# Performance work log

Hardware: AMD Instinct MI355X
Metric: run time of the kernel (lower is better)

Reference implementation:

```python
import jax, jax.numpy as jnp
from jax import lax
import numpy as np

B, L, E, D, A, M, V, T = 64, 196, 2048, 512, 512, 512, 30000, 21


def setup_inputs() -> dict:
    key = jax.random.key(0)
    ks = jax.random.split(key, 22)
    s = 0.02
    encoder_out = jax.random.normal(ks[0], (B, L, E), jnp.float32)
    captions = jax.random.randint(ks[1], (B, T), 0, V, dtype=jnp.int32)
    lens = jax.random.randint(ks[2], (B,), 2, T + 1, dtype=jnp.int32)
    caption_lengths = jnp.sort(lens)[::-1]  # descending, as torch loop requires
    p = {
        'W_enc': jax.random.normal(ks[3], (E, A)) * s, 'b_enc': jnp.zeros((A,)),
        'W_dec': jax.random.normal(ks[4], (D, A)) * s, 'b_dec': jnp.zeros((A,)),
        'w_att': jax.random.normal(ks[5], (A, 1)) * s, 'b_att': jnp.zeros((1,)),
        'emb': jax.random.uniform(ks[6], (V, M), minval=-0.1, maxval=0.1),
        'W_ih': jax.random.normal(ks[7], (M + E, 4 * D)) * s, 'b_ih': jnp.zeros((4 * D,)),
        'W_hh': jax.random.normal(ks[8], (D, 4 * D)) * s, 'b_hh': jnp.zeros((4 * D,)),
        'W_h0': jax.random.normal(ks[9], (E, D)) * s, 'b_h0': jnp.zeros((D,)),
        'W_c0': jax.random.normal(ks[10], (E, D)) * s, 'b_c0': jnp.zeros((D,)),
        'W_beta': jax.random.normal(ks[11], (D, E)) * s, 'b_beta': jnp.zeros((E,)),
        'W_fc': jax.random.uniform(ks[12], (D, V), minval=-0.1, maxval=0.1), 'b_fc': jnp.zeros((V,)),
    }
    return {'encoder_out': encoder_out, 'captions': captions,
            'caption_lengths': caption_lengths, **p}


def reference(encoder_out, captions, caption_lengths,
              W_enc, b_enc, W_dec, b_dec, w_att, b_att, emb,
              W_ih, b_ih, W_hh, b_hh, W_h0, b_h0, W_c0, b_c0,
              W_beta, b_beta, W_fc, b_fc):
    max_len = captions.shape[1] - 1  # teacher forcing: predict y_1..y_T
    x_emb = emb[captions]            # [B,T,M]  (dropout = identity in eval)

    mean_enc = encoder_out.mean(axis=1)
    h0 = jnp.tanh(mean_enc @ W_h0 + b_h0)
    c0 = jnp.tanh(mean_enc @ W_c0 + b_c0)

    # enc projection is constant across timesteps -> hoist out of the loop
    e_proj = encoder_out @ W_enc + b_enc  # [B,L,A]

    # mask[b,t] = (caption_lengths[b]-1) > t  (valid only because lens sorted desc,
    # matching the torch batch_t truncation exactly)
    mask = (caption_lengths[:, None] - 1) > jnp.arange(max_len)[None, :]

    def step(carry, xs):
        h, c = carry
        emb_t, m = xs  # [B,M], [B]
        d = h @ W_dec + b_dec                                   # [B,A]
        energy = (jax.nn.relu(e_proj + d[:, None, :]) @ w_att)[..., 0] + b_att[0]  # [B,L]
        alpha = jax.nn.softmax(energy, axis=1)
        ctx = jnp.einsum('ble,bl->be', encoder_out, alpha)      # [B,E]
        gate = jax.nn.sigmoid(h @ W_beta + b_beta)
        x = jnp.concatenate([emb_t, gate * ctx], axis=1)        # [B,M+E]
        gates = x @ W_ih + b_ih + h @ W_hh + b_hh               # [B,4D]
        i, f, g, o = jnp.split(gates, 4, axis=1)
        c_new = jax.nn.sigmoid(f) * c + jax.nn.sigmoid(i) * jnp.tanh(g)
        h_new = jax.nn.sigmoid(o) * jnp.tanh(c_new)
        pred = h_new @ W_fc + b_fc                              # [B,V]
        mf = m[:, None].astype(pred.dtype)
        return (h_new, c_new), (pred * mf, alpha * mf)

    xs = (jnp.swapaxes(x_emb[:, :max_len, :], 0, 1), mask.T)    # time-major
    _, (preds, alphas) = lax.scan(step, (h0, c0), xs)
    predictions = jnp.swapaxes(preds, 0, 1)                     # [B,max_len,V]
    alphas = jnp.swapaxes(alphas, 0, 1)                         # [B,max_len,L]
    return predictions, alphas
```

## Files before the change

### kernel.cpp

```cpp
#include <hip/hip_runtime.h>
#include <math.h>

namespace {

constexpr int NB  = 64;
constexpr int NL  = 196;
constexpr int NE  = 2048;
constexpr int ND  = 512;
constexpr int NA  = 512;
constexpr int NM  = 512;
constexpr int NV  = 30000;
constexpr int NT  = 21;
constexpr int NML = 20;
constexpr int NG  = 4 * ND;
constexpr int KXG = NM + NE + ND;
constexpr int KSPL = 8, KSL = KXG / KSPL;
constexpr int NALL = ND + NE + NV;
constexpr int OFF_GATE = ND;
constexpr int OFF_PRED = ND + NE;

constexpr size_t WS_MEAN = 0;
constexpr size_t WS_C0   = WS_MEAN + (size_t)NB * NE;
constexpr size_t WS_C1   = WS_C0   + (size_t)NB * ND;
constexpr size_t WS_D    = WS_C1   + (size_t)NB * ND;
constexpr size_t WS_GATE = WS_D    + (size_t)NB * NA;
constexpr size_t WS_EN   = WS_GATE + (size_t)NB * NE;
constexpr size_t WS_CNT  = WS_EN   + (size_t)NB * NL;
constexpr size_t WS_PP   = WS_CNT  + 64;
constexpr size_t WS_SHB  = WS_PP   + (size_t)1048576;
constexpr size_t SH_HB0  = 0;
constexpr size_t SH_HB1  = SH_HB0  + (size_t)NB * ND;
constexpr size_t SH_XEMB = SH_HB1  + (size_t)NB * ND;
constexpr size_t SH_GCTX = SH_XEMB + (size_t)NML * NB * NM;
constexpr size_t SH_EPROJ= SH_GCTX + (size_t)NB * NE;
constexpr size_t SH_WET  = SH_EPROJ+ (size_t)NB * NL * NA;
constexpr size_t SH_WIHX = SH_WET  + (size_t)NA * NE;
constexpr size_t SH_WALL = SH_WIHX + (size_t)NG * KXG;
constexpr size_t SH_ENCBF= SH_WALL + (size_t)NALL * ND;
constexpr size_t SH_END  = SH_ENCBF+ (size_t)NB * NL * NE;
constexpr size_t BYTES_ENC = WS_SHB * 4 + SH_END * 2;

typedef __attribute__((ext_vector_type(8))) short short8v;
typedef __attribute__((ext_vector_type(4))) float f32x4;

__device__ __forceinline__ float sigmoidf_(float x) { return 1.f / (1.f + expf(-x)); }
__device__ __forceinline__ short f2bf(float f) {
  unsigned u = __float_as_uint(f);
  return (short)((u + 0x7FFFu + ((u >> 16) & 1u)) >> 16);
}
__device__ __forceinline__ float bf2f(short s) {
  return __uint_as_float(((unsigned)(unsigned short)s) << 16);
}


__device__ __forceinline__ void gload16(const short* g, short* l) {
  __builtin_amdgcn_global_load_lds(
      (const __attribute__((address_space(1))) unsigned int*)(g),
      (__attribute__((address_space(3))) unsigned int*)(l), 16, 0, 0);
}

template <int R>
__device__ __forceinline__ void stage_direct(const short* __restrict__ src, int ldK,
                                             int rowClamp, short* lds, int tid) {
  int wv = tid >> 6, lane = tid & 63;
  int sub = lane >> 3;
  int kb  = (lane & 7) ^ sub;
#pragma unroll
  for (int g = wv; g < R / 8; g += 4) {
    int row = g * 8 + sub;
    int r = row < rowClamp ? row : rowClamp;
    gload16(src + (size_t)r * ldK + (kb << 3), lds + g * 512);
  }
}

template <int R>
__device__ __forceinline__ void stage_f32cvt(const float* __restrict__ src, int ldK,
                                             short* lds, int tid) {
#pragma unroll
  for (int cidx = tid; cidx < R * 8; cidx += 256) {
    int row = cidx >> 3, kb = cidx & 7;
    const float* p = src + (size_t)row * ldK + kb * 8;
    float4 x = *(const float4*)p;
    float4 y = *(const float4*)(p + 4);
    short8v s;
    s[0] = f2bf(x.x); s[1] = f2bf(x.y); s[2] = f2bf(x.z); s[3] = f2bf(x.w);
    s[4] = f2bf(y.x); s[5] = f2bf(y.y); s[6] = f2bf(y.z); s[7] = f2bf(y.w);
    *(short8v*)(lds + row * 64 + ((kb ^ (row & 7)) << 3)) = s;
  }
}

template <int FM, int FN>
__device__ __forceinline__ void mma_tiles(const short* ldsA, const short* ldsB,
                                          int wr, int wc, int lane, f32x4 acc[FM][FN]) {
  int l15 = lane & 15;
#pragma unroll
  for (int kk = 0; kk < 2; ++kk) {
    int kb0 = kk * 4 + (lane >> 4);
    short8v a[FM], b[FN];
#pragma unroll
    for (int m = 0; m < FM; ++m) {
      int row = wr * FM * 16 + m * 16 + l15;
      a[m] = *(const short8v*)(ldsA + row * 64 + ((kb0 ^ (row & 7)) << 3));
    }
#pragma unroll
    for (int n = 0; n < FN; ++n) {
      int row = wc * FN * 16 + n * 16 + l15;
      b[n] = *(const short8v*)(ldsB + row * 64 + ((kb0 ^ (row & 7)) << 3));
    }
#pragma unroll
    for (int m = 0; m < FM; ++m)
#pragma unroll
      for (int n = 0; n < FN; ++n)
        acc[m][n] = __builtin_amdgcn_mfma_f32_16x16x32_bf16(a[m], b[n], acc[m][n], 0, 0, 0);
  }
}


template <bool PERM>
__global__ __launch_bounds__(256) void k_tcvt(const float* __restrict__ src, int Ks, int Ns,
                                              short* __restrict__ dst, int ldDst, int kOff) {
  __shared__ float tbuf[32][33];
  int n0 = blockIdx.x * 32, k0 = blockIdx.y * 32;
  int tx = threadIdx.x, ty = threadIdx.y;
#pragma unroll
  for (int i = 0; i < 32; i += 8) {
    int k = k0 + ty + i, n = n0 + tx;
    tbuf[ty + i][tx] = (k < Ks && n < Ns) ? src[(size_t)k * Ns + n] : 0.f;
  }
  __syncthreads();
#pragma unroll
  for (int i = 0; i < 32; i += 8) {
    int n = n0 + ty + i, k = k0 + tx;
    if (n < Ns && k < Ks) {
      int nd = PERM ? (((n & 511) << 2) | (n >> 9)) : n;
      dst[(size_t)nd * ldDst + kOff + k] = f2bf(tbuf[tx][ty + i]);
    }
  }
}

template <bool BF>
__global__ __launch_bounds__(256) void k_prep(const float* __restrict__ enc,
                                              short* __restrict__ encbf,
                                              float* __restrict__ mean_enc) {
  int b = blockIdx.y;
  int e = blockIdx.x * 256 + threadIdx.x;
  const float* p = enc + (size_t)b * NL * NE + e;
  short* q = encbf + (size_t)b * NL * NE + e;
  float s = 0.f;
  for (int l = 0; l < NL; ++l) {
    float v = p[(size_t)l * NE];
    s += v;
    if (BF) q[(size_t)l * NE] = f2bf(v);
  }
  mean_enc[(size_t)b * NE + e] = s * (1.f / NL);
}

__global__ void k_xemb(const int* __restrict__ caps, const float* __restrict__ emb,
                       short* __restrict__ xemb) {
  int i = blockIdx.x * 256 + threadIdx.x;
  int m = i & (NM - 1), b = (i >> 9) & (NB - 1), t = i >> 15;
  xemb[i] = f2bf(emb[(size_t)caps[b * NT + t] * NM + m]);
}

__global__ void k_init0(const float* __restrict__ mean_enc, const float* __restrict__ W_h0,
                        const float* __restrict__ W_c0, float* __restrict__ PP) {
  int idx = blockIdx.x * 256 + threadIdx.x;
  int ks = blockIdx.y;
  int b = idx >> 10, jh = idx & 1023, half = jh >> 9, j = jh & 511;
  const float* W = half ? W_c0 : W_h0;
  const float* mp = mean_enc + (size_t)b * NE + ks * 128;
  const float* Wp = W + (size_t)(ks * 128) * ND + j;
  float acc = 0.f;
#pragma unroll 4
  for (int k = 0; k < 128; ++k) acc = fmaf(mp[k], Wp[(size_t)k * ND], acc);
  PP[(size_t)ks * 65536 + idx] = acc;
}

__global__ void k_init1(const float* __restrict__ PP, const float* __restrict__ b_h0,
                        const float* __restrict__ b_c0, float* __restrict__ c0,
                        short* __restrict__ hb0) {
  int idx = blockIdx.x * 256 + threadIdx.x;
  int b = idx >> 9, j = idx & 511;
  float ah = b_h0[j], ac = b_c0[j];
  for (int s = 0; s < 16; ++s) {
    const float* p = PP + (size_t)s * 65536 + b * 1024;
    ah += p[j]; ac += p[512 + j];
  }
  c0[idx] = tanhf(ac);
  hb0[idx] = f2bf(tanhf(ah));
}

template <bool BF>
__global__ __launch_bounds__(256) void k_eproj(const float* __restrict__ enc,
                                               const short* __restrict__ encbf,
                                               const short* __restrict__ We_t,
                                               const float* __restrict__ b_enc,
                                               short* __restrict__ e_proj) {
  constexpr int FM = 4, FN = 4;
  __shared__ short ldsA[128 * 64], ldsB[128 * 64];
  int p = blockIdx.x;
  int l = (p & 7) * 49 + (p >> 3);
  int bn = (l & 3) * 128, bm = (l >> 2) * 128;
  int tid = threadIdx.x, lane = tid & 63, wave = tid >> 6, wr = wave >> 1, wc = wave & 1;
  f32x4 acc[FM][FN];
#pragma unroll
  for (int m = 0; m < FM; ++m)
#pragma unroll
    for (int n = 0; n < FN; ++n) acc[m][n] = (f32x4){0.f, 0.f, 0.f, 0.f};
  for (int k0 = 0; k0 < NE; k0 += 64) {
    __syncthreads();
    if (BF) stage_direct<128>(encbf + (size_t)bm * NE + k0, NE, 127, ldsA, tid);
    else    stage_f32cvt<128>(enc + (size_t)bm * NE + k0, NE, ldsA, tid);
    stage_direct<128>(We_t + (size_t)bn * NE + k0, NE, 127, ldsB, tid);
    __syncthreads();
    mma_tiles<FM, FN>(ldsA, ldsB, wr, wc, lane, acc);
  }
#pragma unroll
  for (int m = 0; m < FM; ++m)
#pragma unroll
    for (int n = 0; n < FN; ++n) {
      int col = bn + wc * FN * 16 + n * 16 + (lane & 15);
      float bias = b_enc[col];
#pragma unroll
      for (int r = 0; r < 4; ++r) {
        int row = bm + wr * FM * 16 + m * 16 + (lane >> 4) * 4 + r;
        e_proj[(size_t)row * NA + col] = f2bf(acc[m][n][r] + bias);
      }
    }
}

__global__ __launch_bounds__(256) void k_hgemm(const short* __restrict__ h_bf,
                                               const short* __restrict__ Wall_t,
                                               const float* __restrict__ b_dec,
                                               const float* __restrict__ b_beta,
                                               const float* __restrict__ b_fc,
                                               const int* __restrict__ clen,
                                               float* __restrict__ d_buf,
                                               float* __restrict__ gatebuf,
                                               float* __restrict__ preds, int t) {
  constexpr int FM = 2, FN = 2;
  __shared__ short ldsA[64 * 64], ldsB[64 * 64];
  int bn = blockIdx.x * 64;
  int tid = threadIdx.x, lane = tid & 63, wave = tid >> 6, wr = wave >> 1, wc = wave & 1;
  int rowClampB = NALL - 1 - bn; if (rowClampB > 63) rowClampB = 63;
  f32x4 acc[FM][FN];
#pragma unroll
  for (int m = 0; m < FM; ++m)
#pragma unroll
    for (int n = 0; n < FN; ++n) acc[m][n] = (f32x4){0.f, 0.f, 0.f, 0.f};
  for (int k0 = 0; k0 < ND; k0 += 64) {
    __syncthreads();
    stage_direct<64>(h_bf + k0, ND, 63, ldsA, tid);
    stage_direct<64>(Wall_t + (size_t)bn * ND + k0, ND, rowClampB, ldsB, tid);
    __syncthreads();
    mma_tiles<FM, FN>(ldsA, ldsB, wr, wc, lane, acc);
  }
#pragma unroll
  for (int m = 0; m < FM; ++m)
#pragma unroll
    for (int r = 0; r < 4; ++r) {
      int row = wr * FM * 16 + m * 16 + (lane >> 4) * 4 + r;
      float mf = ((clen[row] - 1) > t) ? 1.f : 0.f;
#pragma unroll
      for (int n = 0; n < FN; ++n) {
        int col = bn + wc * FN * 16 + n * 16 + (lane & 15);
        float a = acc[m][n][r];
        if (bn < OFF_GATE) {
          d_buf[(size_t)row * NA + col] = a + b_dec[col];
        } else if (bn < OFF_PRED) {
          int e = col - OFF_GATE;
          gatebuf[(size_t)row * NE + e] = sigmoidf_(a + b_beta[e]);
        } else {
          int v = col - OFF_PRED;
          if (v < NV) preds[((size_t)row * NML + t) * NV + v] = mf * (a + b_fc[v]);
        }
      }
    }
}


__global__ __launch_bounds__(256) void k_energy(const short* __restrict__ e_proj,
                                                const float* __restrict__ d_buf,
                                                const float* __restrict__ w_att,
                                                const float* __restrict__ b_att,
                                                float* __restrict__ energy) {
  int tid = threadIdx.x, wave = tid >> 6, lane = tid & 63;
  int row = blockIdx.x * 4 + wave;
  int b = row / NL;
  short8v ev = *(const short8v*)(e_proj + (size_t)row * NA + lane * 8);
  const float* dp = d_buf + (size_t)b * NA + lane * 8;
  float4 d0 = *(const float4*)dp, d1 = *(const float4*)(dp + 4);
  const float* wp = w_att + lane * 8;
  float4 w0 = *(const float4*)wp, w1 = *(const float4*)(wp + 4);
  float dd[8] = {d0.x, d0.y, d0.z, d0.w, d1.x, d1.y, d1.z, d1.w};
  float ww[8] = {w0.x, w0.y, w0.z, w0.w, w1.x, w1.y, w1.z, w1.w};
  float acc = 0.f;
#pragma unroll
  for (int i = 0; i < 8; ++i) {
    float v = bf2f(ev[i]) + dd[i];
    acc = fmaf(fmaxf(v, 0.f), ww[i], acc);
  }
#pragma unroll
  for (int off = 32; off; off >>= 1) acc += __shfl_down(acc, off);
  if (lane == 0) energy[row] = acc + b_att[0];
}

template <bool BF>
__global__ __launch_bounds__(256) void k_ctx(const short* __restrict__ encbf,
                                             const float* __restrict__ encf,
                                             const float* __restrict__ energy,
                                             const float* __restrict__ gatebuf,
                                             const int* __restrict__ clen,
                                             short* __restrict__ gctx,
                                             float* __restrict__ alphas_out, int t) {
  int b = blockIdx.y, e0 = blockIdx.x * 512, tid = threadIdx.x;
  __shared__ float al[NL];
  __shared__ float red[8];
  int wave = tid >> 6, lane = tid & 63;
  float v = (tid < NL) ? energy[b * NL + tid] : -INFINITY;
  float mx = v;
#pragma unroll
  for (int off = 32; off; off >>= 1) mx = fmaxf(mx, __shfl_down(mx, off));
  if (lane == 0) red[wave] = mx;
  __syncthreads();
  if (tid == 0) red[0] = fmaxf(fmaxf(red[0], red[1]), fmaxf(red[2], red[3]));
  __syncthreads();
  mx = red[0];
  float ex = (tid < NL) ? expf(v - mx) : 0.f;
  float sm = ex;
#pragma unroll
  for (int off = 32; off; off >>= 1) sm += __shfl_down(sm, off);
  if (lane == 0) red[4 + wave] = sm;
  __syncthreads();
  if (tid == 0) red[0] = 1.f / (red[4] + red[5] + red[6] + red[7]);
  __syncthreads();
  float alv = ex * red[0];
  if (tid < NL) {
    al[tid] = alv;
    if (blockIdx.x == 0) {
      float mf = ((clen[b] - 1) > t) ? 1.f : 0.f;
      alphas_out[((size_t)b * NML + t) * NL + tid] = alv * mf;
    }
  }
  __syncthreads();
  float cx0 = 0.f, cx1 = 0.f;
  if (BF) {
    const unsigned* p = (const unsigned*)(encbf + (size_t)b * NL * NE + e0) + tid;
#pragma unroll 4
    for (int l = 0; l < NL; ++l) {
      unsigned u = p[(size_t)l * (NE / 2)];
      cx0 = fmaf(al[l], bf2f((short)(u & 0xffffu)), cx0);
      cx1 = fmaf(al[l], bf2f((short)(u >> 16)), cx1);
    }
  } else {
    const float* p = encf + (size_t)b * NL * NE + e0 + 2 * tid;
#pragma unroll 4
    for (int l = 0; l < NL; ++l) {
      float2 u = *(const float2*)(p + (size_t)l * NE);
      cx0 = fmaf(al[l], u.x, cx0);
      cx1 = fmaf(al[l], u.y, cx1);
    }
  }
  int e = e0 + 2 * tid;
  const float* gp = gatebuf + (size_t)b * NE + e;
  unsigned out = (unsigned)(unsigned short)f2bf(cx0 * gp[0]) |
                 ((unsigned)(unsigned short)f2bf(cx1 * gp[1]) << 16);
  *(unsigned*)(gctx + (size_t)b * NE + e) = out;
}

__global__ __launch_bounds__(256) void k_gates(const short* __restrict__ xemb_t,
                                               const short* __restrict__ gctx,
                                               const short* __restrict__ h_prev,
                                               const short* __restrict__ Wihx_t,
                                               float* __restrict__ P) {
  constexpr int FM = 2, FN = 2;
  __shared__ short ldsA[64 * 64], ldsB[64 * 64];
  int bn = blockIdx.x * 64, ks = blockIdx.y;
  int tid = threadIdx.x, lane = tid & 63, wave = tid >> 6, wr = wave >> 1, wc = wave & 1;
  f32x4 acc[FM][FN];
#pragma unroll
  for (int m = 0; m < FM; ++m)
#pragma unroll
    for (int n = 0; n < FN; ++n) acc[m][n] = (f32x4){0.f, 0.f, 0.f, 0.f};
  int kend = (ks + 1) * KSL;
  for (int k0 = ks * KSL; k0 < kend; k0 += 64) {
    const short* asrc; int aldk;
    if (k0 < NM)           { asrc = xemb_t + k0;              aldk = NM; }
    else if (k0 < NM + NE) { asrc = gctx + (k0 - NM);         aldk = NE; }
    else                   { asrc = h_prev + (k0 - NM - NE);  aldk = ND; }
    __syncthreads();
    stage_direct<64>(asrc, aldk, 63, ldsA, tid);
    stage_direct<64>(Wihx_t + (size_t)bn * KXG + k0, KXG, 63, ldsB, tid);
    __syncthreads();
    mma_tiles<FM, FN>(ldsA, ldsB, wr, wc, lane, acc);
  }
#pragma unroll
  for (int m = 0; m < FM; ++m)
#pragma unroll
    for (int n = 0; n < FN; ++n) {
      int col = bn + wc * FN * 16 + n * 16 + (lane & 15);
#pragma unroll
      for (int r = 0; r < 4; ++r) {
        int row = wr * FM * 16 + m * 16 + (lane >> 4) * 4 + r;
        P[((size_t)ks * NB + row) * NG + col] = acc[m][n][r];
      }
    }
}

__global__ void k_lstm(const float* __restrict__ P, const float* __restrict__ b_ih,
                       const float* __restrict__ b_hh, const float* __restrict__ c_prev,
                       float* __restrict__ c_next, short* __restrict__ h_next) {
  int idx = blockIdx.x * 256 + threadIdx.x;
  int b = idx >> 9, j = idx & (ND - 1);
  float gi = b_ih[j] + b_hh[j];
  float gf = b_ih[j + ND] + b_hh[j + ND];
  float gg = b_ih[j + 2 * ND] + b_hh[j + 2 * ND];
  float go = b_ih[j + 3 * ND] + b_hh[j + 3 * ND];
#pragma unroll
  for (int s = 0; s < KSPL; ++s) {
    float4 v = *(const float4*)&P[((size_t)s * NB + b) * NG + j * 4];
    gi += v.x; gf += v.y; gg += v.z; go += v.w;
  }
  float cn = sigmoidf_(gf) * c_prev[idx] + sigmoidf_(gi) * tanhf(gg);
  float hn = sigmoidf_(go) * tanhf(cn);
  c_next[idx] = cn;
  h_next[idx] = f2bf(hn);
}

}

extern "C" void kernel_launch(void* const* d_in, const int* in_sizes, int n_in,
                              void* d_out, int out_size, void* d_ws, size_t ws_size,
                              hipStream_t stream) {
  (void)in_sizes; (void)n_in; (void)out_size;
  const float* enc    = (const float*)d_in[0];
  const int*   caps   = (const int*)d_in[1];
  const int*   clen   = (const int*)d_in[2];
  const float* W_enc  = (const float*)d_in[3];
  const float* b_enc  = (const float*)d_in[4];
  const float* W_dec  = (const float*)d_in[5];
  const float* b_dec  = (const float*)d_in[6];
  const float* w_att  = (const float*)d_in[7];
  const float* b_att  = (const float*)d_in[8];
  const float* emb    = (const float*)d_in[9];
  const float* W_ih   = (const float*)d_in[10];
  const float* b_ih   = (const float*)d_in[11];
  const float* W_hh   = (const float*)d_in[12];
  const float* b_hh   = (const float*)d_in[13];
  const float* W_h0   = (const float*)d_in[14];
  const float* b_h0   = (const float*)d_in[15];
  const float* W_c0   = (const float*)d_in[16];
  const float* b_c0   = (const float*)d_in[17];
  const float* W_beta = (const float*)d_in[18];
  const float* b_beta = (const float*)d_in[19];
  const float* W_fc   = (const float*)d_in[20];
  const float* b_fc   = (const float*)d_in[21];

  float* ws     = (float*)d_ws;
  float* preds  = (float*)d_out;
  float* alphas = preds + (size_t)NB * NML * NV;

  float* mean_enc = ws + WS_MEAN;
  float* cbuf[2]  = {ws + WS_C0, ws + WS_C1};
  float* d_buf    = ws + WS_D;
  float* gatebuf  = ws + WS_GATE;
  float* energy   = ws + WS_EN;
  float* PP       = ws + WS_PP;
  short* shb      = (short*)(ws + WS_SHB);
  short* hbuf[2]  = {shb + SH_HB0, shb + SH_HB1};
  short* xemb     = shb + SH_XEMB;
  short* gctx     = shb + SH_GCTX;
  short* e_proj   = shb + SH_EPROJ;
  short* We_t     = shb + SH_WET;
  short* Wihx_t   = shb + SH_WIHX;
  short* Wall_t   = shb + SH_WALL;
  short* encbf    = shb + SH_ENCBF;
  const bool use_bf = ws_size >= BYTES_ENC;

  k_tcvt<false><<<dim3(NA / 32, NE / 32), dim3(32, 8), 0, stream>>>(W_enc, NE, NA, We_t, NE, 0);
  k_tcvt<true><<<dim3(NG / 32, (NM + NE) / 32), dim3(32, 8), 0, stream>>>(
      W_ih, NM + NE, NG, Wihx_t, KXG, 0);
  k_tcvt<true><<<dim3(NG / 32, ND / 32), dim3(32, 8), 0, stream>>>(
      W_hh, ND, NG, Wihx_t, KXG, NM + NE);
  k_tcvt<false><<<dim3(NA / 32, ND / 32), dim3(32, 8), 0, stream>>>(W_dec, ND, NA, Wall_t, ND, 0);
  k_tcvt<false><<<dim3(NE / 32, ND / 32), dim3(32, 8), 0, stream>>>(
      W_beta, ND, NE, Wall_t + (size_t)OFF_GATE * ND, ND, 0);
  k_tcvt<false><<<dim3((NV + 31) / 32, ND / 32), dim3(32, 8), 0, stream>>>(
      W_fc, ND, NV, Wall_t + (size_t)OFF_PRED * ND, ND, 0);
  if (use_bf)
    k_prep<true><<<dim3(NE / 256, NB), 256, 0, stream>>>(enc, encbf, mean_enc);
  else
    k_prep<false><<<dim3(NE / 256, NB), 256, 0, stream>>>(enc, encbf, mean_enc);
  k_xemb<<<(NML * NB * NM) / 256, 256, 0, stream>>>(caps, emb, xemb);

  k_init0<<<dim3(256, 16), 256, 0, stream>>>(mean_enc, W_h0, W_c0, PP);
  k_init1<<<(NB * ND) / 256, 256, 0, stream>>>(PP, b_h0, b_c0, cbuf[0], hbuf[0]);
  if (use_bf)
    k_eproj<true><<<392, 256, 0, stream>>>(enc, encbf, We_t, b_enc, e_proj);
  else
    k_eproj<false><<<392, 256, 0, stream>>>(enc, encbf, We_t, b_enc, e_proj);
  k_hgemm<<<OFF_PRED / 64, 256, 0, stream>>>(hbuf[0], Wall_t, b_dec, b_beta, b_fc, clen,
                                             d_buf, gatebuf, preds, 0);

  for (int t = 0; t < NML; ++t) {
    short* h_prev = hbuf[t & 1];
    short* h_next = hbuf[1 - (t & 1)];
    float* c_prev = cbuf[t & 1];
    float* c_next = cbuf[1 - (t & 1)];
    k_energy<<<(NB * NL) / 4, 256, 0, stream>>>(e_proj, d_buf, w_att, b_att, energy);
    if (use_bf)
      k_ctx<true><<<dim3(NE / 512, NB), 256, 0, stream>>>(encbf, enc, energy, gatebuf,
                                                          clen, gctx, alphas, t);
    else
      k_ctx<false><<<dim3(NE / 512, NB), 256, 0, stream>>>(encbf, enc, energy, gatebuf,
                                                           clen, gctx, alphas, t);
    k_gates<<<dim3(NG / 64, KSPL), 256, 0, stream>>>(xemb + (size_t)t * NB * NM, gctx,
                                                     h_prev, Wihx_t, PP);
    k_lstm<<<(NB * ND) / 256, 256, 0, stream>>>(PP, b_ih, b_hh, c_prev, c_next, h_next);
    k_hgemm<<<(NALL + 63) / 64, 256, 0, stream>>>(h_next, Wall_t, b_dec, b_beta, b_fc,
                                                  clen, d_buf, gatebuf, preds, t);
  }
}
```

Measured before the change: 1.157 ms.

## Batch vocab projection across timesteps and fold h·W_hh into hidden GEMM

All hidden states are now stored in one buffer, so the 30000-wide output projection runs once after the loop as a single 1280-row GEMM with 128x128 tiles. Previously it ran every timestep with only 64 rows. The h·W_hh product moves out of the split-K gates GEMM into the per-step hidden GEMM, alongside the decoder and beta projections, and is added in the LSTM cell kernel. This makes the W_fc weight reads far more reusable and shrinks the recurrent critical path. The cost is more workspace for the stored hidden states and a separate transposed W_fc buffer.

```diff
diff --git a/kernel.cpp b/kernel.cpp
--- a/kernel.cpp
+++ b/kernel.cpp
@@ -13,30 +13,30 @@
 constexpr int NT  = 21;
 constexpr int NML = 20;
 constexpr int NG  = 4 * ND;
-constexpr int KXG = NM + NE + ND;
+constexpr int KXG = NM + NE;
 constexpr int KSPL = 8, KSL = KXG / KSPL;
-constexpr int NALL = ND + NE + NV;
+constexpr int NDG = ND + NE + NG;
 constexpr int OFF_GATE = ND;
-constexpr int OFF_PRED = ND + NE;
+constexpr int OFF_HWHH = ND + NE;
 
 constexpr size_t WS_MEAN = 0;
 constexpr size_t WS_C0   = WS_MEAN + (size_t)NB * NE;
 constexpr size_t WS_C1   = WS_C0   + (size_t)NB * ND;
 constexpr size_t WS_D    = WS_C1   + (size_t)NB * ND;
 constexpr size_t WS_GATE = WS_D    + (size_t)NB * NA;
-constexpr size_t WS_EN   = WS_GATE + (size_t)NB * NE;
-constexpr size_t WS_CNT  = WS_EN   + (size_t)NB * NL;
-constexpr size_t WS_PP   = WS_CNT  + 64;
+constexpr size_t WS_HWHH = WS_GATE + (size_t)NB * NE;
+constexpr size_t WS_EN   = WS_HWHH + (size_t)NB * NG;
+constexpr size_t WS_PP   = WS_EN   + (size_t)NB * NL;
 constexpr size_t WS_SHB  = WS_PP   + (size_t)1048576;
-constexpr size_t SH_HB0  = 0;
-constexpr size_t SH_HB1  = SH_HB0  + (size_t)NB * ND;
-constexpr size_t SH_XEMB = SH_HB1  + (size_t)NB * ND;
+constexpr size_t SH_HALL = 0;
+constexpr size_t SH_XEMB = SH_HALL + (size_t)(NML + 1) * NB * ND;
 constexpr size_t SH_GCTX = SH_XEMB + (size_t)NML * NB * NM;
 constexpr size_t SH_EPROJ= SH_GCTX + (size_t)NB * NE;
 constexpr size_t SH_WET  = SH_EPROJ+ (size_t)NB * NL * NA;
 constexpr size_t SH_WIHX = SH_WET  + (size_t)NA * NE;
 constexpr size_t SH_WALL = SH_WIHX + (size_t)NG * KXG;
-constexpr size_t SH_ENCBF= SH_WALL + (size_t)NALL * ND;
+constexpr size_t SH_WFC  = SH_WALL + (size_t)NDG * ND;
+constexpr size_t SH_ENCBF= SH_WFC  + (size_t)NV * ND;
 constexpr size_t SH_END  = SH_ENCBF+ (size_t)NB * NL * NE;
 constexpr size_t BYTES_ENC = WS_SHB * 4 + SH_END * 2;
 
@@ -178,7 +178,7 @@
 
 __global__ void k_init1(const float* __restrict__ PP, const float* __restrict__ b_h0,
                         const float* __restrict__ b_c0, float* __restrict__ c0,
-                        short* __restrict__ hb0) {
+                        short* __restrict__ h0) {
   int idx = blockIdx.x * 256 + threadIdx.x;
   int b = idx >> 9, j = idx & 511;
   float ah = b_h0[j], ac = b_c0[j];
@@ -187,7 +187,7 @@
     ah += p[j]; ac += p[512 + j];
   }
   c0[idx] = tanhf(ac);
-  hb0[idx] = f2bf(tanhf(ah));
+  h0[idx] = f2bf(tanhf(ah));
 }
 
 template <bool BF>
@@ -229,20 +229,17 @@
     }
 }
 
-__global__ __launch_bounds__(256) void k_hgemm(const short* __restrict__ h_bf,
-                                               const short* __restrict__ Wall_t,
-                                               const float* __restrict__ b_dec,
-                                               const float* __restrict__ b_beta,
-                                               const float* __restrict__ b_fc,
-                                               const int* __restrict__ clen,
-                                               float* __restrict__ d_buf,
-                                               float* __restrict__ gatebuf,
-                                               float* __restrict__ preds, int t) {
+__global__ __launch_bounds__(256) void k_hgemm_dg(const short* __restrict__ h_bf,
+                                                  const short* __restrict__ Wall_t,
+                                                  const float* __restrict__ b_dec,
+                                                  const float* __restrict__ b_beta,
+                                                  float* __restrict__ d_buf,
+                                                  float* __restrict__ gatebuf,
+                                                  float* __restrict__ hWhh) {
   constexpr int FM = 2, FN = 2;
   __shared__ short ldsA[64 * 64], ldsB[64 * 64];
   int bn = blockIdx.x * 64;
   int tid = threadIdx.x, lane = tid & 63, wave = tid >> 6, wr = wave >> 1, wc = wave & 1;
-  int rowClampB = NALL - 1 - bn; if (rowClampB > 63) rowClampB = 63;
   f32x4 acc[FM][FN];
 #pragma unroll
   for (int m = 0; m < FM; ++m)
@@ -251,7 +248,7 @@
   for (int k0 = 0; k0 < ND; k0 += 64) {
     __syncthreads();
     stage_direct<64>(h_bf + k0, ND, 63, ldsA, tid);
-    stage_direct<64>(Wall_t + (size_t)bn * ND + k0, ND, rowClampB, ldsB, tid);
+    stage_direct<64>(Wall_t + (size_t)bn * ND + k0, ND, 63, ldsB, tid);
     __syncthreads();
     mma_tiles<FM, FN>(ldsA, ldsB, wr, wc, lane, acc);
   }
@@ -260,19 +257,17 @@
 #pragma unroll
     for (int r = 0; r < 4; ++r) {
       int row = wr * FM * 16 + m * 16 + (lane >> 4) * 4 + r;
-      float mf = ((clen[row] - 1) > t) ? 1.f : 0.f;
 #pragma unroll
       for (int n = 0; n < FN; ++n) {
         int col = bn + wc * FN * 16 + n * 16 + (lane & 15);
         float a = acc[m][n][r];
         if (bn < OFF_GATE) {
           d_buf[(size_t)row * NA + col] = a + b_dec[col];
-        } else if (bn < OFF_PRED) {
+        } else if (bn < OFF_HWHH) {
           int e = col - OFF_GATE;
           gatebuf[(size_t)row * NE + e] = sigmoidf_(a + b_beta[e]);
         } else {
-          int v = col - OFF_PRED;
-          if (v < NV) preds[((size_t)row * NML + t) * NV + v] = mf * (a + b_fc[v]);
+          hWhh[(size_t)row * NG + (col - OFF_HWHH)] = a;
         }
       }
     }
@@ -370,7 +365,6 @@
 
 __global__ __launch_bounds__(256) void k_gates(const short* __restrict__ xemb_t,
                                                const short* __restrict__ gctx,
-                                               const short* __restrict__ h_prev,
                                                const short* __restrict__ Wihx_t,
                                                float* __restrict__ P) {
   constexpr int FM = 2, FN = 2;
@@ -385,9 +379,8 @@
   int kend = (ks + 1) * KSL;
   for (int k0 = ks * KSL; k0 < kend; k0 += 64) {
     const short* asrc; int aldk;
-    if (k0 < NM)           { asrc = xemb_t + k0;              aldk = NM; }
-    else if (k0 < NM + NE) { asrc = gctx + (k0 - NM);         aldk = NE; }
-    else                   { asrc = h_prev + (k0 - NM - NE);  aldk = ND; }
+    if (k0 < NM) { asrc = xemb_t + k0;      aldk = NM; }
+    else         { asrc = gctx + (k0 - NM); aldk = NE; }
     __syncthreads();
     stage_direct<64>(asrc, aldk, 63, ldsA, tid);
     stage_direct<64>(Wihx_t + (size_t)bn * KXG + k0, KXG, 63, ldsB, tid);
@@ -407,15 +400,17 @@
     }
 }
 
-__global__ void k_lstm(const float* __restrict__ P, const float* __restrict__ b_ih,
-                       const float* __restrict__ b_hh, const float* __restrict__ c_prev,
-                       float* __restrict__ c_next, short* __restrict__ h_next) {
+__global__ void k_lstm(const float* __restrict__ P, const float* __restrict__ hWhh,
+                       const float* __restrict__ b_ih, const float* __restrict__ b_hh,
+                       const float* __restrict__ c_prev, float* __restrict__ c_next,
+                       short* __restrict__ h_next) {
   int idx = blockIdx.x * 256 + threadIdx.x;
   int b = idx >> 9, j = idx & (ND - 1);
-  float gi = b_ih[j] + b_hh[j];
-  float gf = b_ih[j + ND] + b_hh[j + ND];
-  float gg = b_ih[j + 2 * ND] + b_hh[j + 2 * ND];
-  float go = b_ih[j + 3 * ND] + b_hh[j + 3 * ND];
+  float4 hw = *(const float4*)&hWhh[(size_t)b * NG + j * 4];
+  float gi = b_ih[j] + b_hh[j] + hw.x;
+  float gf = b_ih[j + ND] + b_hh[j + ND] + hw.y;
+  float gg = b_ih[j + 2 * ND] + b_hh[j + 2 * ND] + hw.z;
+  float go = b_ih[j + 3 * ND] + b_hh[j + 3 * ND] + hw.w;
 #pragma unroll
   for (int s = 0; s < KSPL; ++s) {
     float4 v = *(const float4*)&P[((size_t)s * NB + b) * NG + j * 4];
@@ -425,6 +420,52 @@
   float hn = sigmoidf_(go) * tanhf(cn);
   c_next[idx] = cn;
   h_next[idx] = f2bf(hn);
+}
+
+__global__ __launch_bounds__(256) void k_pred(const short* __restrict__ h_all1,
+                                              const short* __restrict__ Wfc_t,
+                                              const float* __restrict__ b_fc,
+                                              const int* __restrict__ clen,
+                                              float* __restrict__ preds) {
+  constexpr int FM = 4, FN = 4;
+  constexpr int NT_M = 10, NT_N = (NV + 127) / 128;
+  constexpr int TOT = NT_M * NT_N;
+  __shared__ short ldsA[128 * 64], ldsB[128 * 64];
+  int p = blockIdx.x;
+  int q = TOT / 8, r8 = TOT % 8;
+  int xcd = p & 7, i = p >> 3;
+  int l = (xcd < r8 ? xcd * (q + 1) : r8 * (q + 1) + (xcd - r8) * q) + i;
+  int bm = (l % NT_M) * 128, bn = (l / NT_M) * 128;
+  int tid = threadIdx.x, lane = tid & 63, wave = tid >> 6, wr = wave >> 1, wc = wave & 1;
+  int rowClampB = NV - 1 - bn; if (rowClampB > 127) rowClampB = 127;
+  f32x4 acc[FM][FN];
+#pragma unroll
+  for (int m = 0; m < FM; ++m)
+#pragma unroll
+    for (int n = 0; n < FN; ++n) acc[m][n] = (f32x4){0.f, 0.f, 0.f, 0.f};
+  for (int k0 = 0; k0 < ND; k0 += 64) {
+    __syncthreads();
+    stage_direct<128>(h_all1 + (size_t)bm * ND + k0, ND, 127, ldsA, tid);
+    stage_direct<128>(Wfc_t + (size_t)bn * ND + k0, ND, rowClampB, ldsB, tid);
+    __syncthreads();
+    mma_tiles<FM, FN>(ldsA, ldsB, wr, wc, lane, acc);
+  }
+#pragma unroll
+  for (int m = 0; m < FM; ++m)
+#pragma unroll
+    for (int n = 0; n < FN; ++n) {
+      int col = bn + wc * FN * 16 + n * 16 + (lane & 15);
+      if (col < NV) {
+        float bias = b_fc[col];
+#pragma unroll
+        for (int r = 0; r < 4; ++r) {
+          int row = bm + wr * FM * 16 + m * 16 + (lane >> 4) * 4 + r;
+          int t = row >> 6, b = row & 63;
+          float mf = ((clen[b] - 1) > t) ? 1.f : 0.f;
+          preds[((size_t)b * NML + t) * NV + col] = mf * (acc[m][n][r] + bias);
+        }
+      }
+    }
 }
 
 }
@@ -464,29 +505,31 @@
   float* cbuf[2]  = {ws + WS_C0, ws + WS_C1};
   float* d_buf    = ws + WS_D;
   float* gatebuf  = ws + WS_GATE;
+  float* hWhh     = ws + WS_HWHH;
   float* energy   = ws + WS_EN;
   float* PP       = ws + WS_PP;
   short* shb      = (short*)(ws + WS_SHB);
-  short* hbuf[2]  = {shb + SH_HB0, shb + SH_HB1};
+  short* h_all    = shb + SH_HALL;
   short* xemb     = shb + SH_XEMB;
   short* gctx     = shb + SH_GCTX;
   short* e_proj   = shb + SH_EPROJ;
   short* We_t     = shb + SH_WET;
   short* Wihx_t   = shb + SH_WIHX;
   short* Wall_t   = shb + SH_WALL;
+  short* Wfc_t    = shb + SH_WFC;
   short* encbf    = shb + SH_ENCBF;
   const bool use_bf = ws_size >= BYTES_ENC;
 
   k_tcvt<false><<<dim3(NA / 32, NE / 32), dim3(32, 8), 0, stream>>>(W_enc, NE, NA, We_t, NE, 0);
-  k_tcvt<true><<<dim3(NG / 32, (NM + NE) / 32), dim3(32, 8), 0, stream>>>(
-      W_ih, NM + NE, NG, Wihx_t, KXG, 0);
-  k_tcvt<true><<<dim3(NG / 32, ND / 32), dim3(32, 8), 0, stream>>>(
-      W_hh, ND, NG, Wihx_t, KXG, NM + NE);
+  k_tcvt<true><<<dim3(NG / 32, KXG / 32), dim3(32, 8), 0, stream>>>(
+      W_ih, KXG, NG, Wihx_t, KXG, 0);
   k_tcvt<false><<<dim3(NA / 32, ND / 32), dim3(32, 8), 0, stream>>>(W_dec, ND, NA, Wall_t, ND, 0);
   k_tcvt<false><<<dim3(NE / 32, ND / 32), dim3(32, 8), 0, stream>>>(
       W_beta, ND, NE, Wall_t + (size_t)OFF_GATE * ND, ND, 0);
+  k_tcvt<true><<<dim3(NG / 32, ND / 32), dim3(32, 8), 0, stream>>>(
+      W_hh, ND, NG, Wall_t + (size_t)OFF_HWHH * ND, ND, 0);
   k_tcvt<false><<<dim3((NV + 31) / 32, ND / 32), dim3(32, 8), 0, stream>>>(
-      W_fc, ND, NV, Wall_t + (size_t)OFF_PRED * ND, ND, 0);
+      W_fc, ND, NV, Wfc_t, ND, 0);
   if (use_bf)
     k_prep<true><<<dim3(NE / 256, NB), 256, 0, stream>>>(enc, encbf, mean_enc);
   else
@@ -494,17 +537,16 @@
   k_xemb<<<(NML * NB * NM) / 256, 256, 0, stream>>>(caps, emb, xemb);
 
   k_init0<<<dim3(256, 16), 256, 0, stream>>>(mean_enc, W_h0, W_c0, PP);
-  k_init1<<<(NB * ND) / 256, 256, 0, stream>>>(PP, b_h0, b_c0, cbuf[0], hbuf[0]);
+  k_init1<<<(NB * ND) / 256, 256, 0, stream>>>(PP, b_h0, b_c0, cbuf[0], h_all);
   if (use_bf)
     k_eproj<true><<<392, 256, 0, stream>>>(enc, encbf, We_t, b_enc, e_proj);
   else
     k_eproj<false><<<392, 256, 0, stream>>>(enc, encbf, We_t, b_enc, e_proj);
-  k_hgemm<<<OFF_PRED / 64, 256, 0, stream>>>(hbuf[0], Wall_t, b_dec, b_beta, b_fc, clen,
-                                             d_buf, gatebuf, preds, 0);
+  k_hgemm_dg<<<NDG / 64, 256, 0, stream>>>(h_all, Wall_t, b_dec, b_beta,
+                                           d_buf, gatebuf, hWhh);
 
   for (int t = 0; t < NML; ++t) {
-    short* h_prev = hbuf[t & 1];
-    short* h_next = hbuf[1 - (t & 1)];
+    short* h_next = h_all + (size_t)(t + 1) * NB * ND;
     float* c_prev = cbuf[t & 1];
     float* c_next = cbuf[1 - (t & 1)];
     k_energy<<<(NB * NL) / 4, 256, 0, stream>>>(e_proj, d_buf, w_att, b_att, energy);
@@ -515,9 +557,13 @@
       k_ctx<false><<<dim3(NE / 512, NB), 256, 0, stream>>>(encbf, enc, energy, gatebuf,
                                                            clen, gctx, alphas, t);
     k_gates<<<dim3(NG / 64, KSPL), 256, 0, stream>>>(xemb + (size_t)t * NB * NM, gctx,
-                                                     h_prev, Wihx_t, PP);
-    k_lstm<<<(NB * ND) / 256, 256, 0, stream>>>(PP, b_ih, b_hh, c_prev, c_next, h_next);
-    k_hgemm<<<(NALL + 63) / 64, 256, 0, stream>>>(h_next, Wall_t, b_dec, b_beta, b_fc,
-                                                  clen, d_buf, gatebuf, preds, t);
-  }
-}
+                                                     Wihx_t, PP);
+    k_lstm<<<(NB * ND) / 256, 256, 0, stream>>>(PP, hWhh, b_ih, b_hh, c_prev, c_next,
+                                                h_next);
+    if (t + 1 < NML)
+      k_hgemm_dg<<<NDG / 64, 256, 0, stream>>>(h_next, Wall_t, b_dec, b_beta,
+                                               d_buf, gatebuf, hWhh);
+  }
+  k_pred<<<10 * ((NV + 127) / 128), 256, 0, stream>>>(h_all + (size_t)NB * ND, Wfc_t,
+                                                      b_fc, clen, preds);
+}
```

Result: no change. 1.173 ms (+1.4%).

## Fold h·W_hh into the fused h-GEMM and shrink the gates GEMM K dimension

Applied to the files above, without the earlier changes.

The recurrent h@W_hh product moves out of the per-step gates GEMM and into the k_hgemm that already multiplies h by W_dec, W_beta and W_fc. Its result is stored in a new hWhh buffer that the LSTM cell kernel adds in. This shortens the K loop of k_gates (from M+E+D to M+E) on the critical serial path and reuses the h tile already staged in the h-GEMM. In exchange the h-GEMM grows by 4D output columns and the LSTM kernel reads an extra fp32 buffer. The cell-kernel read assumes hWhh uses the same interleaved column layout as the transposed-converted W_ih block.

```diff
diff --git a/kernel.cpp b/kernel.cpp
--- a/kernel.cpp
+++ b/kernel.cpp
@@ -13,20 +13,24 @@
 constexpr int NT  = 21;
 constexpr int NML = 20;
 constexpr int NG  = 4 * ND;
-constexpr int KXG = NM + NE + ND;
+constexpr int KXG = NM + NE;
 constexpr int KSPL = 8, KSL = KXG / KSPL;
 constexpr int NALL = ND + NE + NV;
 constexpr int OFF_GATE = ND;
 constexpr int OFF_PRED = ND + NE;
+
+constexpr int OFF_HWHH2 = ND + NE;
+constexpr int OFF_PRED2 = ND + NE + NG;
+constexpr int NALL2 = ND + NE + NG + NV;
 
 constexpr size_t WS_MEAN = 0;
 constexpr size_t WS_C0   = WS_MEAN + (size_t)NB * NE;
 constexpr size_t WS_C1   = WS_C0   + (size_t)NB * ND;
 constexpr size_t WS_D    = WS_C1   + (size_t)NB * ND;
 constexpr size_t WS_GATE = WS_D    + (size_t)NB * NA;
-constexpr size_t WS_EN   = WS_GATE + (size_t)NB * NE;
-constexpr size_t WS_CNT  = WS_EN   + (size_t)NB * NL;
-constexpr size_t WS_PP   = WS_CNT  + 64;
+constexpr size_t WS_HWHH = WS_GATE + (size_t)NB * NE;
+constexpr size_t WS_EN   = WS_HWHH + (size_t)NB * NG;
+constexpr size_t WS_PP   = WS_EN   + (size_t)NB * NL;
 constexpr size_t WS_SHB  = WS_PP   + (size_t)1048576;
 constexpr size_t SH_HB0  = 0;
 constexpr size_t SH_HB1  = SH_HB0  + (size_t)NB * ND;
@@ -36,7 +40,7 @@
 constexpr size_t SH_WET  = SH_EPROJ+ (size_t)NB * NL * NA;
 constexpr size_t SH_WIHX = SH_WET  + (size_t)NA * NE;
 constexpr size_t SH_WALL = SH_WIHX + (size_t)NG * KXG;
-constexpr size_t SH_ENCBF= SH_WALL + (size_t)NALL * ND;
+constexpr size_t SH_ENCBF= SH_WALL + (size_t)NALL2 * ND;
 constexpr size_t SH_END  = SH_ENCBF+ (size_t)NB * NL * NE;
 constexpr size_t BYTES_ENC = WS_SHB * 4 + SH_END * 2;
 
@@ -237,12 +241,13 @@
                                                const int* __restrict__ clen,
                                                float* __restrict__ d_buf,
                                                float* __restrict__ gatebuf,
+                                               float* __restrict__ hWhh,
                                                float* __restrict__ preds, int t) {
   constexpr int FM = 2, FN = 2;
   __shared__ short ldsA[64 * 64], ldsB[64 * 64];
   int bn = blockIdx.x * 64;
   int tid = threadIdx.x, lane = tid & 63, wave = tid >> 6, wr = wave >> 1, wc = wave & 1;
-  int rowClampB = NALL - 1 - bn; if (rowClampB > 63) rowClampB = 63;
+  int rowClampB = NALL2 - 1 - bn; if (rowClampB > 63) rowClampB = 63;
   f32x4 acc[FM][FN];
 #pragma unroll
   for (int m = 0; m < FM; ++m)
@@ -267,11 +272,13 @@
         float a = acc[m][n][r];
         if (bn < OFF_GATE) {
           d_buf[(size_t)row * NA + col] = a + b_dec[col];
-        } else if (bn < OFF_PRED) {
+        } else if (bn < OFF_HWHH2) {
           int e = col - OFF_GATE;
           gatebuf[(size_t)row * NE + e] = sigmoidf_(a + b_beta[e]);
+        } else if (bn < OFF_PRED2) {
+          hWhh[(size_t)row * NG + (col - OFF_HWHH2)] = a;
         } else {
-          int v = col - OFF_PRED;
+          int v = col - OFF_PRED2;
           if (v < NV) preds[((size_t)row * NML + t) * NV + v] = mf * (a + b_fc[v]);
         }
       }
@@ -370,7 +377,6 @@
 
 __global__ __launch_bounds__(256) void k_gates(const short* __restrict__ xemb_t,
                                                const short* __restrict__ gctx,
-                                               const short* __restrict__ h_prev,
                                                const short* __restrict__ Wihx_t,
                                                float* __restrict__ P) {
   constexpr int FM = 2, FN = 2;
@@ -385,9 +391,8 @@
   int kend = (ks + 1) * KSL;
   for (int k0 = ks * KSL; k0 < kend; k0 += 64) {
     const short* asrc; int aldk;
-    if (k0 < NM)           { asrc = xemb_t + k0;              aldk = NM; }
-    else if (k0 < NM + NE) { asrc = gctx + (k0 - NM);         aldk = NE; }
-    else                   { asrc = h_prev + (k0 - NM - NE);  aldk = ND; }
+    if (k0 < NM) { asrc = xemb_t + k0;      aldk = NM; }
+    else         { asrc = gctx + (k0 - NM); aldk = NE; }
     __syncthreads();
     stage_direct<64>(asrc, aldk, 63, ldsA, tid);
     stage_direct<64>(Wihx_t + (size_t)bn * KXG + k0, KXG, 63, ldsB, tid);
@@ -407,15 +412,17 @@
     }
 }
 
-__global__ void k_lstm(const float* __restrict__ P, const float* __restrict__ b_ih,
-                       const float* __restrict__ b_hh, const float* __restrict__ c_prev,
-                       float* __restrict__ c_next, short* __restrict__ h_next) {
+__global__ void k_lstm(const float* __restrict__ P, const float* __restrict__ hWhh,
+                       const float* __restrict__ b_ih, const float* __restrict__ b_hh,
+                       const float* __restrict__ c_prev, float* __restrict__ c_next,
+                       short* __restrict__ h_next) {
   int idx = blockIdx.x * 256 + threadIdx.x;
   int b = idx >> 9, j = idx & (ND - 1);
-  float gi = b_ih[j] + b_hh[j];
-  float gf = b_ih[j + ND] + b_hh[j + ND];
-  float gg = b_ih[j + 2 * ND] + b_hh[j + 2 * ND];
-  float go = b_ih[j + 3 * ND] + b_hh[j + 3 * ND];
+  float4 hw = *(const float4*)&hWhh[(size_t)b * NG + j * 4];
+  float gi = b_ih[j] + b_hh[j] + hw.x;
+  float gf = b_ih[j + ND] + b_hh[j + ND] + hw.y;
+  float gg = b_ih[j + 2 * ND] + b_hh[j + 2 * ND] + hw.z;
+  float go = b_ih[j + 3 * ND] + b_hh[j + 3 * ND] + hw.w;
 #pragma unroll
   for (int s = 0; s < KSPL; ++s) {
     float4 v = *(const float4*)&P[((size_t)s * NB + b) * NG + j * 4];
@@ -464,6 +471,7 @@
   float* cbuf[2]  = {ws + WS_C0, ws + WS_C1};
   float* d_buf    = ws + WS_D;
   float* gatebuf  = ws + WS_GATE;
+  float* hWhh     = ws + WS_HWHH;
   float* energy   = ws + WS_EN;
   float* PP       = ws + WS_PP;
   short* shb      = (short*)(ws + WS_SHB);
@@ -478,15 +486,15 @@
   const bool use_bf = ws_size >= BYTES_ENC;
 
   k_tcvt<false><<<dim3(NA / 32, NE / 32), dim3(32, 8), 0, stream>>>(W_enc, NE, NA, We_t, NE, 0);
-  k_tcvt<true><<<dim3(NG / 32, (NM + NE) / 32), dim3(32, 8), 0, stream>>>(
-      W_ih, NM + NE, NG, Wihx_t, KXG, 0);
-  k_tcvt<true><<<dim3(NG / 32, ND / 32), dim3(32, 8), 0, stream>>>(
-      W_hh, ND, NG, Wihx_t, KXG, NM + NE);
+  k_tcvt<true><<<dim3(NG / 32, KXG / 32), dim3(32, 8), 0, stream>>>(
+      W_ih, KXG, NG, Wihx_t, KXG, 0);
   k_tcvt<false><<<dim3(NA / 32, ND / 32), dim3(32, 8), 0, stream>>>(W_dec, ND, NA, Wall_t, ND, 0);
   k_tcvt<false><<<dim3(NE / 32, ND / 32), dim3(32, 8), 0, stream>>>(
       W_beta, ND, NE, Wall_t + (size_t)OFF_GATE * ND, ND, 0);
+  k_tcvt<true><<<dim3(NG / 32, ND / 32), dim3(32, 8), 0, stream>>>(
+      W_hh, ND, NG, Wall_t + (size_t)OFF_HWHH2 * ND, ND, 0);
   k_tcvt<false><<<dim3((NV + 31) / 32, ND / 32), dim3(32, 8), 0, stream>>>(
-      W_fc, ND, NV, Wall_t + (size_t)OFF_PRED * ND, ND, 0);
+      W_fc, ND, NV, Wall_t + (size_t)OFF_PRED2 * ND, ND, 0);
   if (use_bf)
     k_prep<true><<<dim3(NE / 256, NB), 256, 0, stream>>>(enc, encbf, mean_enc);
   else
@@ -499,8 +507,8 @@
     k_eproj<true><<<392, 256, 0, stream>>>(enc, encbf, We_t, b_enc, e_proj);
   else
     k_eproj<false><<<392, 256, 0, stream>>>(enc, encbf, We_t, b_enc, e_proj);
-  k_hgemm<<<OFF_PRED / 64, 256, 0, stream>>>(hbuf[0], Wall_t, b_dec, b_beta, b_fc, clen,
-                                             d_buf, gatebuf, preds, 0);
+  k_hgemm<<<OFF_PRED2 / 64, 256, 0, stream>>>(hbuf[0], Wall_t, b_dec, b_beta, b_fc, clen,
+                                              d_buf, gatebuf, hWhh, preds, 0);
 
   for (int t = 0; t < NML; ++t) {
     short* h_prev = hbuf[t & 1];
@@ -515,9 +523,11 @@
       k_ctx<false><<<dim3(NE / 512, NB), 256, 0, stream>>>(encbf, enc, energy, gatebuf,
                                                            clen, gctx, alphas, t);
     k_gates<<<dim3(NG / 64, KSPL), 256, 0, stream>>>(xemb + (size_t)t * NB * NM, gctx,
-                                                     h_prev, Wihx_t, PP);
-    k_lstm<<<(NB * ND) / 256, 256, 0, stream>>>(PP, b_ih, b_hh, c_prev, c_next, h_next);
-    k_hgemm<<<(NALL + 63) / 64, 256, 0, stream>>>(h_next, Wall_t, b_dec, b_beta, b_fc,
-                                                  clen, d_buf, gatebuf, preds, t);
-  }
-}
+                                                     Wihx_t, PP);
+    k_lstm<<<(NB * ND) / 256, 256, 0, stream>>>(PP, hWhh, b_ih, b_hh, c_prev, c_next,
+                                                h_next);
+    (void)h_prev;
+    k_hgemm<<<(NALL2 + 63) / 64, 256, 0, stream>>>(h_next, Wall_t, b_dec, b_beta, b_fc,
+                                                   clen, d_buf, gatebuf, hWhh, preds, t);
+  }
+}
```

Result: no change. 1.158 ms (+0.1%).
